# Performance work log

Measured on AMD Instinct MI355X. Metric: run time of the kernel, lower is better.

Reference implementation:

```python
import jax, jax.numpy as jnp
import numpy as np
import math

N_HEADS = 32
N_KV_HEADS = 8
HEAD_DIM = 64
THETA = 10000.0
NEG_INF = -1e9


def _rope_cos_sin(seq_len, dim, dtype=jnp.float32):
    # freqs over even indices, matching torch.arange(0, dim, 2)/dim
    freqs = 1.0 / (THETA ** (jnp.arange(0, dim, 2, dtype=jnp.float32) / dim))  # [dim/2]
    angles = jnp.arange(seq_len, dtype=jnp.float32)[:, None] * freqs[None, :]  # [S, dim/2]
    return jnp.cos(angles).astype(dtype), jnp.sin(angles).astype(dtype)


def _apply_rope(x, cos, sin):
    # x: [B, S, H, D]; pairs (x[...,2i], x[...,2i+1]) rotated as complex numbers
    xr = x[..., 0::2]
    xi = x[..., 1::2]
    # broadcast cos/sin [S, D/2] -> [1, S, 1, D/2]
    c = cos[None, :, None, :]
    s = sin[None, :, None, :]
    or_ = xr * c - xi * s
    oi_ = xr * s + xi * c
    # interleave back: [..., D/2, 2] -> [..., D]
    return jnp.stack([or_, oi_], axis=-1).reshape(x.shape)


def setup_inputs() -> dict:
    key = jax.random.key(0)
    ks = jax.random.split(key, 5)
    B, S, D = 2, 2048, 2048
    KV_D = N_KV_HEADS * HEAD_DIM
    x = jax.random.normal(ks[0], (B, S, D), dtype=jnp.float32)
    sc = 1.0 / math.sqrt(D)
    wq = jax.random.normal(ks[1], (D, D), dtype=jnp.float32) * sc
    wk = jax.random.normal(ks[2], (D, KV_D), dtype=jnp.float32) * sc
    wv = jax.random.normal(ks[3], (D, KV_D), dtype=jnp.float32) * sc
    wo = jax.random.normal(ks[4], (D, D), dtype=jnp.float32) * sc
    # additive causal mask [1, 1, S, S]
    causal = jnp.tril(jnp.ones((S, S), dtype=bool))
    mask = jnp.where(causal, 0.0, NEG_INF).astype(jnp.float32)[None, None]
    return {"x": x, "mask": mask, "wq": wq, "wk": wk, "wv": wv, "wo": wo}


def reference(x, mask, wq, wk, wv, wo):
    B, S, D = x.shape
    n_rep = N_HEADS // N_KV_HEADS
    q = (x @ wq).reshape(B, S, N_HEADS, HEAD_DIM)
    k = (x @ wk).reshape(B, S, N_KV_HEADS, HEAD_DIM)
    v = (x @ wv).reshape(B, S, N_KV_HEADS, HEAD_DIM)
    cos, sin = _rope_cos_sin(S, HEAD_DIM)
    q = _apply_rope(q, cos, sin)
    k = _apply_rope(k, cos, sin)
    # GQA: repeat_interleave kv heads along head dim
    k = jnp.repeat(k, n_rep, axis=2)  # [B, S, H, D]
    v = jnp.repeat(v, n_rep, axis=2)
    scores = jnp.einsum("bqhd,bkhd->bhqk", q, k) / math.sqrt(HEAD_DIM)
    scores = scores + mask
    probs = jax.nn.softmax(scores.astype(jnp.float32), axis=-1).astype(q.dtype)
    out = jnp.einsum("bhqk,bkhd->bqhd", probs, v).reshape(B, S, N_HEADS * HEAD_DIM)
    return out @ wo
```

## Files before the change

### kernel.cpp

```cpp
#include <hip/hip_runtime.h>
#include <hip/hip_bf16.h>


#define S_LEN 2048
#define BATCH 2
#define D_MODEL 2048
#define NH 32
#define NKV 8
#define HD 64
#define KV_D (NKV * HD)
#define QKV_N (D_MODEL + 2 * KV_D)

typedef __attribute__((ext_vector_type(8))) short short8;
typedef __attribute__((ext_vector_type(4))) float float4v;
typedef __attribute__((ext_vector_type(16))) float f32x16;
typedef __attribute__((ext_vector_type(2))) unsigned uint2v;

typedef __attribute__((address_space(1))) const unsigned int gu32;
typedef __attribute__((address_space(3))) unsigned int lu32;

#if __has_builtin(__builtin_amdgcn_exp2f)
#define PEXP(x) __builtin_amdgcn_exp2f(x)
#else
#define PEXP(x) __expf((x) * 0.69314718f)
#endif
#define QSCALE 0.18033688f

__device__ __forceinline__ float bf2f(unsigned short u) {
    unsigned x = ((unsigned)u) << 16;
    return __builtin_bit_cast(float, x);
}
__device__ __forceinline__ unsigned short f2bf(float f) {
    unsigned u = __builtin_bit_cast(unsigned, f);
    unsigned r = (u + 0x7fffu + ((u >> 16) & 1u)) >> 16;
    return (unsigned short)r;
}

__device__ __forceinline__ unsigned cvt_pk_bf16(float a, float b) {
    unsigned r;
    asm("v_cvt_pk_bf16_f32 %0, %1, %2" : "=v"(r) : "v"(a), "v"(b));
    return r;
}

__device__ __forceinline__ void pl32swap(unsigned a, unsigned b,
                                         unsigned& x, unsigned& y) {
#if __has_builtin(__builtin_amdgcn_permlane32_swap)
    uint2v r = __builtin_amdgcn_permlane32_swap(a, b, false, false);
    x = r[0];
    y = r[1];
#else
    unsigned pa = (unsigned)__shfl_xor((int)a, 32);
    unsigned pb = (unsigned)__shfl_xor((int)b, 32);
    bool lo = (threadIdx.x & 63) < 32;
    x = lo ? a : pb;
    y = lo ? pa : b;
#endif
}

__global__ __launch_bounds__(256) void prep(const float* __restrict__ x,
                                            const float* __restrict__ wq,
                                            const float* __restrict__ wk,
                                            const float* __restrict__ wv,
                                            const float* __restrict__ wo,
                                            unsigned short* __restrict__ xb,
                                            unsigned short* __restrict__ wqkvT,
                                            unsigned short* __restrict__ woT) {
    __shared__ unsigned short t[32 * 33];
    const int bx = blockIdx.x;
    if (bx >= 10240) {
        long i = ((long)(bx - 10240) * 256 + threadIdx.x) * 4;
        const long n = (long)BATCH * S_LEN * D_MODEL;
        if (i + 3 >= n) return;
        const float4v v = *(const float4v*)&x[i];
        unsigned short o[4];
        o[0] = f2bf(v[0]); o[1] = f2bf(v[1]); o[2] = f2bf(v[2]); o[3] = f2bf(v[3]);
        *(__attribute__((ext_vector_type(4))) short*)&xb[i] =
            *(__attribute__((ext_vector_type(4))) short*)o;
        return;
    }
    const float* in;
    unsigned short* out;
    int N, nb, kb;
    if (bx < 4096) {
        in = wq; out = wqkvT; N = 2048;
        nb = (bx & 63) * 32; kb = (bx >> 6) * 32;
    } else if (bx < 5120) {
        const int i2 = bx - 4096;
        in = wk; out = wqkvT + (long)D_MODEL * D_MODEL; N = 512;
        nb = (i2 & 15) * 32; kb = (i2 >> 4) * 32;
    } else if (bx < 6144) {
        const int i2 = bx - 5120;
        in = wv; out = wqkvT + (long)(D_MODEL + KV_D) * D_MODEL; N = 512;
        nb = (i2 & 15) * 32; kb = (i2 >> 4) * 32;
    } else {
        const int i2 = bx - 6144;
        in = wo; out = woT; N = 2048;
        nb = (i2 & 63) * 32; kb = (i2 >> 6) * 32;
    }
    const int c = threadIdx.x & 31, rr = threadIdx.x >> 5;
#pragma unroll
    for (int it = 0; it < 4; ++it) {
        int r = it * 8 + rr;
        t[c * 33 + r] = f2bf(in[(long)(kb + r) * N + nb + c]);
    }
    __syncthreads();
#pragma unroll
    for (int it = 0; it < 4; ++it) {
        int r = it * 8 + rr;
        out[(long)(nb + r) * D_MODEL + kb + c] = t[r * 33 + c];
    }
}

template <int TM, bool F32OUT>
__global__ __launch_bounds__(256, TM == 64 ? 4 : 3)
void gemm_sw(const unsigned short* __restrict__ A,
             const unsigned short* __restrict__ BT,
             void* __restrict__ Cv, int M, int N, int K) {
    __shared__ unsigned short As[TM * 64];
    __shared__ unsigned short Bs[128 * 64];
    const int tid = threadIdx.x;
    const int wid = tid >> 6, lane = tid & 63;
    const int l15 = lane & 15, quad = lane >> 4;
    const int wm = (wid >> 1) * (TM / 2), wn = (wid & 1) * 64;

    const int nwg = gridDim.x * gridDim.y;
    const int wgid = blockIdx.y * gridDim.x + blockIdx.x;
    const int v = (wgid & 7) * (nwg >> 3) + (wgid >> 3);
    const int row0 = (v % gridDim.x) * TM, col0 = (v / gridDim.x) * 128;
    constexpr int MI = TM / 32;

    float4v acc[MI][4];
    float4v z;
    z[0] = z[1] = z[2] = z[3] = 0.0f;
    for (int mi = 0; mi < MI; ++mi)
        for (int ni = 0; ni < 4; ++ni) acc[mi][ni] = z;

    const int r_ld = lane >> 3;
    const int swz_ld = ((lane & 7) ^ (lane >> 3)) * 8;
    const int sw = l15 & 7;

    for (int kb = 0; kb < K; kb += 64) {
        __syncthreads();
#pragma unroll
        for (int c = 0; c < 4; ++c) {
            int chunk = c * 4 + wid;
            int r = chunk * 8 + r_ld;
            __builtin_amdgcn_global_load_lds(
                (gu32*)&BT[(long)(col0 + r) * K + kb + swz_ld],
                (lu32*)&Bs[chunk * 512], 16, 0, 0);
            if (c < MI)
                __builtin_amdgcn_global_load_lds(
                    (gu32*)&A[(long)(row0 + r) * K + kb + swz_ld],
                    (lu32*)&As[chunk * 512], 16, 0, 0);
        }
        __syncthreads();
#pragma unroll
        for (int kk = 0; kk < 64; kk += 32) {
            short8 af[MI], bf[4];
#pragma unroll
            for (int i = 0; i < MI; ++i)
                af[i] = *(const short8*)
                    &As[(wm + i * 16 + l15) * 64 + ((((kk >> 3) + quad) ^ sw) << 3)];
#pragma unroll
            for (int i = 0; i < 4; ++i)
                bf[i] = *(const short8*)
                    &Bs[(wn + i * 16 + l15) * 64 + ((((kk >> 3) + quad) ^ sw) << 3)];
#pragma unroll
            for (int mi = 0; mi < MI; ++mi)
#pragma unroll
                for (int ni = 0; ni < 4; ++ni)
                    acc[mi][ni] = __builtin_amdgcn_mfma_f32_16x16x32_bf16(
                        af[mi], bf[ni], acc[mi][ni], 0, 0, 0);
        }
    }
#pragma unroll
    for (int mi = 0; mi < MI; ++mi)
#pragma unroll
        for (int ni = 0; ni < 4; ++ni)
#pragma unroll
            for (int r = 0; r < 4; ++r) {
                int m = row0 + wm + mi * 16 + quad * 4 + r;
                int n = col0 + wn + ni * 16 + l15;
                if (F32OUT)
                    ((float*)Cv)[(long)m * N + n] = acc[mi][ni][r];
                else
                    ((unsigned short*)Cv)[(long)m * N + n] = f2bf(acc[mi][ni][r]);
            }
}

__global__ __launch_bounds__(256) void rope_vtrans(unsigned short* __restrict__ qkv,
                                                   unsigned short* __restrict__ Vt) {
    __shared__ unsigned t[64 * 33];
    const int bx = blockIdx.x, tid = threadIdx.x;
    if (bx < 512) {
        const int i = tid & 31;
        const int row = bx * 8 + (tid >> 5);
        const int s = row & (S_LEN - 1);
        float freq = __expf(-0.28782313f * (float)i);
        float ang = (float)s * freq;
        float c = cosf(ang), sn = sinf(ang);
        unsigned* p = (unsigned*)qkv + ((long)row * QKV_N + 2 * i) / 2;
#pragma unroll
        for (int head = 0; head < 40; ++head) {
            const float qs = (head < 32) ? QSCALE : 1.0f;
            unsigned v = p[head * 32];
            float xr = bf2f((unsigned short)(v & 0xffff));
            float xi = bf2f((unsigned short)(v >> 16));
            unsigned short lo = f2bf((xr * c - xi * sn) * qs);
            unsigned short hi = f2bf((xr * sn + xi * c) * qs);
            p[head * 32] = (unsigned)lo | ((unsigned)hi << 16);
        }
        return;
    }
    const int idx = bx - 512;
    const int st = (idx & 31) * 64, kh = (idx >> 5) & 7, b = idx >> 8;
    {
        const int r2 = tid >> 3, dbase = (tid & 7) * 8;
        const unsigned short* src =
            qkv + ((long)(b * S_LEN + st + 2 * r2)) * QKV_N + D_MODEL + KV_D + kh * HD + dbase;
        short8 lo = *(const short8*)src;
        short8 hi = *(const short8*)(src + QKV_N);
#pragma unroll
        for (int j = 0; j < 8; ++j)
            t[(dbase + j) * 33 + r2] =
                (unsigned)(unsigned short)lo[j] | ((unsigned)(unsigned short)hi[j] << 16);
    }
    __syncthreads();
    {
        const int d = tid >> 2, sb = (tid & 3) * 8;
        unsigned short o[16];
#pragma unroll
        for (int jj = 0; jj < 8; ++jj) {
            unsigned v = t[d * 33 + sb + jj];
            o[2 * jj] = (unsigned short)(v & 0xffff);
            o[2 * jj + 1] = (unsigned short)(v >> 16);
        }
        unsigned short* dst =
            Vt + ((long)((b * 8 + kh) * 64 + d)) * S_LEN + st + sb * 2;
        *(short8*)dst = *(short8*)&o[0];
        *(short8*)(dst + 8) = *(short8*)&o[8];
    }
}

__global__ __launch_bounds__(512, 4) void flash8(const unsigned short* __restrict__ qkv,
                                                 const unsigned short* __restrict__ Vt,
                                                 unsigned short* __restrict__ O) {
    __shared__ unsigned short Ks[4][64 * 64];
    __shared__ unsigned short Vs[4][64 * 64];

    const int tid = threadIdx.x, w = tid >> 6, lane = tid & 63;
    const int g = w & 3, p = w >> 2;
    const int l31 = lane & 31, hi = lane >> 5;
    const int r7 = l31 & 7;

    const int wgid = (blockIdx.z * 32 + blockIdx.y) * 8 + blockIdx.x;
    const int v = (wgid & 7) * 64 + (wgid >> 3);
    const int qtA = v & 7;
    const int h = (v >> 3) & 31;
    const int b = v >> 8;
    const int kh = h >> 2, bkh = b * 8 + kh;

    const int sr = lane >> 3;
    const int sc = ((lane & 7) ^ sr) * 8;
    const unsigned short* Kg =
        qkv + (long)b * S_LEN * QKV_N + D_MODEL + kh * HD + sc;
    const unsigned short* Vg = Vt + ((long)bkh * 64) * S_LEN + sc;

#define STAGE8(pb)                                                                   \
    do {                                                                             \
        const int tt = (pb) + p;                                                     \
        const int bt = tt & 3;                                                       \
        const long kk0 = (long)tt * 64;                                              \
        __builtin_amdgcn_global_load_lds(                                            \
            (gu32*)&Kg[(kk0 + g * 16 + sr) * QKV_N],                                 \
            (lu32*)&Ks[bt][(g * 16) * 64], 16, 0, 0);                                \
        __builtin_amdgcn_global_load_lds(                                            \
            (gu32*)&Kg[(kk0 + g * 16 + 8 + sr) * QKV_N],                             \
            (lu32*)&Ks[bt][(g * 16 + 8) * 64], 16, 0, 0);                            \
        __builtin_amdgcn_global_load_lds(                                            \
            (gu32*)&Vg[(long)(g * 16 + sr) * S_LEN + kk0],                           \
            (lu32*)&Vs[bt][(g * 16) * 64], 16, 0, 0);                                \
        __builtin_amdgcn_global_load_lds(                                            \
            (gu32*)&Vg[(long)(g * 16 + 8 + sr) * S_LEN + kk0],                       \
            (lu32*)&Vs[bt][(g * 16 + 8) * 64], 16, 0, 0);                            \
    } while (0)

    for (int tsel = 0; tsel < 2; ++tsel) {
        const int qt = tsel ? (15 - qtA) : qtA;
        const int row_w = qt * 128 + g * 32;
        const int nkt = 2 * qt + 2;
        const int nss = nkt >> 1;

        short8 aq[4];
        {
            const long qbase = ((long)(b * S_LEN) + row_w + l31) * QKV_N + h * HD + hi * 8;
#pragma unroll
            for (int ks = 0; ks < 4; ++ks) aq[ks] = *(const short8*)&qkv[qbase + ks * 16];
        }

        f32x16 oacc[2] = {};
        float lp = 0.0f;

        STAGE8(0);
        __syncthreads();

        for (int ss = 0; ss < nss; ++ss) {
            const int t = 2 * ss + p;
            const int k0 = t * 64;
            const int bt = t & 3;
            if (2 * ss + 2 < nkt) STAGE8(2 * ss + 2);

            if (row_w + 31 >= k0) {
                const bool mb = (k0 + 63 > row_w);
#pragma unroll
                for (int kb2 = 0; kb2 < 2; ++kb2) {
                    short8 kf[4];
#pragma unroll
                    for (int ks = 0; ks < 4; ++ks)
                        kf[ks] = *(const short8*)
                            &Ks[bt][(kb2 * 32 + l31) * 64 + (((ks * 2 + hi) ^ r7) << 3)];
                    f32x16 s = {};
                    __builtin_amdgcn_s_setprio(1);
#pragma unroll
                    for (int ks = 0; ks < 4; ++ks)
                        s = __builtin_amdgcn_mfma_f32_32x32x16_bf16(kf[ks], aq[ks], s, 0, 0, 0);
                    __builtin_amdgcn_s_setprio(0);

                    const int qrel = row_w + l31 - k0 - kb2 * 32 - 4 * hi;
#pragma unroll
                    for (int r = 0; r < 16; ++r) {
                        float vv = s[r];
                        if (mb && ((r & 3) + 8 * (r >> 2) > qrel)) vv = -1e4f;
                        float pv = PEXP(vv);
                        lp += pv;
                        s[r] = pv;
                    }

#pragma unroll
                    for (int ksl = 0; ksl < 2; ++ksl) {
                        const int gx = ksl * 8;
                        unsigned ca = cvt_pk_bf16(s[gx + 0], s[gx + 1]);
                        unsigned cb = cvt_pk_bf16(s[gx + 2], s[gx + 3]);
                        unsigned cc = cvt_pk_bf16(s[gx + 4], s[gx + 5]);
                        unsigned cd = cvt_pk_bf16(s[gx + 6], s[gx + 7]);
                        unsigned dw0, dw1, dw2, dw3;
                        pl32swap(ca, cc, dw0, dw2);
                        pl32swap(cb, cd, dw1, dw3);
                        union { unsigned u[4]; short8 v8; } pf;
                        pf.u[0] = dw0; pf.u[1] = dw1; pf.u[2] = dw2; pf.u[3] = dw3;
                        const int lc = kb2 * 4 + ksl * 2 + hi;
                        __builtin_amdgcn_s_setprio(1);
#pragma unroll
                        for (int dblk = 0; dblk < 2; ++dblk) {
                            short8 vf = *(const short8*)
                                &Vs[bt][(dblk * 32 + l31) * 64 + ((lc ^ r7) << 3)];
                            oacc[dblk] = __builtin_amdgcn_mfma_f32_32x32x16_bf16(
                                vf, pf.v8, oacc[dblk], 0, 0, 0);
                        }
                        __builtin_amdgcn_s_setprio(0);
                    }
                }
            }
            __syncthreads();
        }

        float* mV = (float*)&Vs[0][0];
        float* mL = (float*)&Ks[2][0];
        if (p == 1) {
#pragma unroll
            for (int dblk = 0; dblk < 2; ++dblk)
#pragma unroll
                for (int r = 0; r < 16; ++r)
                    mV[(g * 32 + dblk * 16 + r) * 64 + lane] = oacc[dblk][r];
            mL[g * 64 + lane] = lp;
        }
        __syncthreads();
        if (p == 0) {
#pragma unroll
            for (int dblk = 0; dblk < 2; ++dblk)
#pragma unroll
                for (int r = 0; r < 16; ++r)
                    oacc[dblk][r] += mV[(g * 32 + dblk * 16 + r) * 64 + lane];
            lp += mL[g * 64 + lane];

            float linv = 1.0f / (lp + __shfl_xor(lp, 32));
            unsigned short* Oe = &Ks[0][0] + g * 2048;
#pragma unroll
            for (int dblk = 0; dblk < 2; ++dblk)
#pragma unroll
                for (int rq = 0; rq < 4; ++rq) {
                    unsigned plo = cvt_pk_bf16(oacc[dblk][rq * 4 + 0] * linv,
                                               oacc[dblk][rq * 4 + 1] * linv);
                    unsigned phi = cvt_pk_bf16(oacc[dblk][rq * 4 + 2] * linv,
                                               oacc[dblk][rq * 4 + 3] * linv);
                    uint2v wv;
                    wv[0] = plo; wv[1] = phi;
                    int e = l31 * 64 + (((rq + 4 * dblk) ^ r7) << 3) + hi * 4;
                    *(uint2v*)&Oe[e] = wv;
                }
#pragma unroll
            for (int i = 0; i < 4; ++i) {
                int q2 = i * 8 + (lane >> 3);
                int e = q2 * 64 + (((lane & 7) ^ (lane >> 3)) << 3);
                short8 ov = *(const short8*)&Oe[e];
                long orow = ((long)(b * S_LEN) + row_w + q2) * D_MODEL + h * HD + (lane & 7) * 8;
                *(short8*)&O[orow] = ov;
            }
        }
        __syncthreads();
    }
#undef STAGE8
}

extern "C" void kernel_launch(void* const* d_in, const int* in_sizes, int n_in,
                              void* d_out, int out_size, void* d_ws, size_t ws_size,
                              hipStream_t stream) {
    const float* x  = (const float*)d_in[0];
    const float* wq = (const float*)d_in[n_in - 4];
    const float* wk = (const float*)d_in[n_in - 3];
    const float* wv = (const float*)d_in[n_in - 2];
    const float* wo = (const float*)d_in[n_in - 1];
    float* out = (float*)d_out;

    unsigned short* ws    = (unsigned short*)d_ws;
    unsigned short* xb    = ws;
    unsigned short* Obuf  = ws;
    unsigned short* qkv   = xb + (long)BATCH * S_LEN * D_MODEL;
    unsigned short* woT   = qkv + (long)BATCH * S_LEN * QKV_N;
    unsigned short* wqkvT = woT + (long)D_MODEL * D_MODEL;
    unsigned short* Vt    = wqkvT;

    const int M = BATCH * S_LEN;

    prep<<<18432, 256, 0, stream>>>(x, wq, wk, wv, wo, xb, wqkvT, woT);

    gemm_sw<128, false><<<dim3(M / 128, QKV_N / 128), 256, 0, stream>>>(
        xb, wqkvT, qkv, M, QKV_N, D_MODEL);

    rope_vtrans<<<1024, 256, 0, stream>>>(qkv, Vt);

    flash8<<<dim3(8, NH, BATCH), 512, 0, stream>>>(qkv, Vt, Obuf);

    gemm_sw<128, true><<<dim3(M / 128, D_MODEL / 128), 256, 0, stream>>>(
        Obuf, woT, out, M, D_MODEL, D_MODEL);
}
```

Measured before the change: 301.0 us.

## Add 256x256 double-buffered GEMM with async LDS loads for QKV projection

Replaces the QKV projection GEMM with a new kernel using 256x256 tiles, 8 waves, and double-buffered shared memory filled by direct global-to-LDS loads. Loads for the next K-step are interleaved with MFMA quadrants under explicit waitcnt and barriers, with priority raised around the MFMA blocks. The grid-swizzle remapping is also removed from the generic GEMM still used for the output projection. The larger tile raises data reuse but gives only 192 workgroups at 2 per CU, which may underfill the GPU. Dropping the swizzle may also hurt cache locality in the output GEMM.

```diff
diff --git a/kernel.cpp b/kernel.cpp
--- a/kernel.cpp
+++ b/kernel.cpp
@@ -122,11 +122,7 @@
     const int wid = tid >> 6, lane = tid & 63;
     const int l15 = lane & 15, quad = lane >> 4;
     const int wm = (wid >> 1) * (TM / 2), wn = (wid & 1) * 64;
-
-    const int nwg = gridDim.x * gridDim.y;
-    const int wgid = blockIdx.y * gridDim.x + blockIdx.x;
-    const int v = (wgid & 7) * (nwg >> 3) + (wgid >> 3);
-    const int row0 = (v % gridDim.x) * TM, col0 = (v / gridDim.x) * 128;
+    const int row0 = blockIdx.x * TM, col0 = blockIdx.y * 128;
     constexpr int MI = TM / 32;
 
     float4v acc[MI][4];
@@ -186,6 +182,144 @@
                 else
                     ((unsigned short*)Cv)[(long)m * N + n] = f2bf(acc[mi][ni][r]);
             }
+}
+
+#define K8 2048
+#define N8 3072
+#define NK8 (K8 / 64)
+
+__device__ __forceinline__ void rd_a8(short8 (&a)[4][2], const unsigned short* L,
+                                      int mh, int wr, int l15, int quad, int sw) {
+#pragma unroll
+    for (int i = 0; i < 4; ++i) {
+        const int ra = mh * 128 + i * 32 + wr * 16 + l15;
+#pragma unroll
+        for (int kk = 0; kk < 2; ++kk)
+            a[i][kk] = *(const short8*)&L[ra * 64 + (((kk * 4 + quad) ^ sw) << 3)];
+    }
+}
+__device__ __forceinline__ void rd_b8(short8 (&b)[2][2], const unsigned short* L,
+                                      int nh, int wc, int l15, int quad, int sw) {
+#pragma unroll
+    for (int j = 0; j < 2; ++j) {
+        const int rb = nh * 128 + j * 64 + wc * 16 + l15;
+#pragma unroll
+        for (int kk = 0; kk < 2; ++kk)
+            b[j][kk] = *(const short8*)&L[rb * 64 + (((kk * 4 + quad) ^ sw) << 3)];
+    }
+}
+__device__ __forceinline__ void mm8(float4v (&acc)[4][2], const short8 (&a)[4][2],
+                                    const short8 (&b)[2][2]) {
+#pragma unroll
+    for (int kk = 0; kk < 2; ++kk)
+#pragma unroll
+        for (int i = 0; i < 4; ++i)
+#pragma unroll
+            for (int j = 0; j < 2; ++j)
+                acc[i][j] = __builtin_amdgcn_mfma_f32_16x16x32_bf16(
+                    a[i][kk], b[j][kk], acc[i][j], 0, 0, 0);
+}
+
+__global__ __launch_bounds__(512, 2)
+void gemm9(const unsigned short* __restrict__ A,
+           const unsigned short* __restrict__ BT,
+           unsigned short* __restrict__ C) {
+    __shared__ unsigned short As[2][256 * 64];
+    __shared__ unsigned short Bs[2][256 * 64];
+    const int tid = threadIdx.x, wid = tid >> 6, lane = tid & 63;
+    const int l15 = lane & 15, quad = lane >> 4, sw = l15 & 7;
+    const int wr = wid >> 2, wc = wid & 3;
+    const int row0 = blockIdx.x * 256, col0 = blockIdx.y * 256;
+
+    const int sr = lane >> 3;
+    const int sc = ((lane & 7) ^ sr) * 8;
+    const unsigned short* Ag = A + (long)(row0 + wid * 8 + sr) * K8 + sc;
+    const unsigned short* Bg = BT + (long)(col0 + wid * 8 + sr) * K8 + sc;
+
+#define STA9(buf, kb, u)                                                \
+    __builtin_amdgcn_global_load_lds(                                   \
+        (gu32*)(Ag + (long)(u) * (64L * K8) + (kb)),                    \
+        (lu32*)&As[buf][((u) * 64 + wid * 8) * 64], 16, 0, 0)
+#define STB9(buf, kb, u)                                                \
+    __builtin_amdgcn_global_load_lds(                                   \
+        (gu32*)(Bg + (long)(u) * (64L * K8) + (kb)),                    \
+        (lu32*)&Bs[buf][((u) * 64 + wid * 8) * 64], 16, 0, 0)
+#define WAITB(n)                                                        \
+    do {                                                                \
+        asm volatile("s_waitcnt vmcnt(" #n ")" ::: "memory");           \
+        __builtin_amdgcn_s_barrier();                                   \
+        asm volatile("" ::: "memory");                                  \
+    } while (0)
+
+    float4v acc[2][2][4][2];
+#pragma unroll
+    for (int mh = 0; mh < 2; ++mh)
+#pragma unroll
+        for (int nh = 0; nh < 2; ++nh)
+#pragma unroll
+            for (int i = 0; i < 4; ++i)
+#pragma unroll
+                for (int j = 0; j < 2; ++j) {
+                    acc[mh][nh][i][j][0] = 0.0f; acc[mh][nh][i][j][1] = 0.0f;
+                    acc[mh][nh][i][j][2] = 0.0f; acc[mh][nh][i][j][3] = 0.0f;
+                }
+
+    STA9(0, 0, 0); STA9(0, 0, 1); STB9(0, 0, 0); STB9(0, 0, 1);
+    STB9(0, 0, 2); STB9(0, 0, 3); STA9(0, 0, 2); STA9(0, 0, 3);
+
+    for (int t = 0; t < NK8; ++t) {
+        const int ct = t & 1, nx = ct ^ 1;
+        const int kb = (t + 1) * 64;
+        const bool more = (t + 1 < NK8);
+        const unsigned short* Al = As[ct];
+        const unsigned short* Bl = Bs[ct];
+        short8 a0[4][2], a1[4][2], b0v[2][2], b1v[2][2];
+
+        WAITB(4);
+        rd_a8(a0, Al, 0, wr, l15, quad, sw);
+        rd_b8(b0v, Bl, 0, wc, l15, quad, sw);
+        if (more) { STA9(nx, kb, 0); STA9(nx, kb, 1); }
+        __builtin_amdgcn_s_setprio(1);
+        mm8(acc[0][0], a0, b0v);
+        __builtin_amdgcn_s_setprio(0);
+
+        if (more) { WAITB(4); } else { WAITB(2); }
+        rd_b8(b1v, Bl, 1, wc, l15, quad, sw);
+        if (more) { STB9(nx, kb, 0); STB9(nx, kb, 1); }
+        __builtin_amdgcn_s_setprio(1);
+        mm8(acc[0][1], a0, b1v);
+        __builtin_amdgcn_s_setprio(0);
+
+        if (more) { WAITB(4); } else { WAITB(0); }
+        rd_a8(a1, Al, 1, wr, l15, quad, sw);
+        if (more) { STB9(nx, kb, 2); STB9(nx, kb, 3); }
+        __builtin_amdgcn_s_setprio(1);
+        mm8(acc[1][0], a1, b0v);
+        __builtin_amdgcn_s_setprio(0);
+
+        if (more) { STA9(nx, kb, 2); STA9(nx, kb, 3); }
+        __builtin_amdgcn_s_setprio(1);
+        mm8(acc[1][1], a1, b1v);
+        __builtin_amdgcn_s_setprio(0);
+    }
+
+#pragma unroll
+    for (int mh = 0; mh < 2; ++mh)
+#pragma unroll
+        for (int nh = 0; nh < 2; ++nh)
+#pragma unroll
+            for (int i = 0; i < 4; ++i)
+#pragma unroll
+                for (int j = 0; j < 2; ++j)
+#pragma unroll
+                    for (int r = 0; r < 4; ++r) {
+                        int m = row0 + mh * 128 + i * 32 + wr * 16 + quad * 4 + r;
+                        int n = col0 + nh * 128 + j * 64 + wc * 16 + l15;
+                        C[(long)m * N8 + n] = f2bf(acc[mh][nh][i][j][r]);
+                    }
+#undef STA9
+#undef STB9
+#undef WAITB
 }
 
 __global__ __launch_bounds__(256) void rope_vtrans(unsigned short* __restrict__ qkv,
@@ -434,8 +568,7 @@
 
     prep<<<18432, 256, 0, stream>>>(x, wq, wk, wv, wo, xb, wqkvT, woT);
 
-    gemm_sw<128, false><<<dim3(M / 128, QKV_N / 128), 256, 0, stream>>>(
-        xb, wqkvT, qkv, M, QKV_N, D_MODEL);
+    gemm9<<<dim3(M / 256, QKV_N / 256), 512, 0, stream>>>(xb, wqkvT, qkv);
 
     rope_vtrans<<<1024, 256, 0, stream>>>(qkv, Vt);
 
```

Result: faster. 287.2 us (-4.6%).
